# Kernel optimization log

Hardware: AMD Instinct MI355X
Metric: run time of the kernel (lower is better)

Reference implementation:

```python
import jax, jax.numpy as jnp
import numpy as np

IN, H, STEPS = 4, 64, 5

def setup_inputs() -> dict:
    key = jax.random.key(0)
    ks = jax.random.split(key, 12)
    s = 1.0 / np.sqrt(H)
    def u(k, shape):
        return jax.random.uniform(k, shape, jnp.float32, -s, s)
    return {
        "x":    jax.random.normal(ks[0], (4096, 512, IN), jnp.float32),
        "Wih0": u(ks[1], (4 * H, IN)),
        "Whh0": u(ks[2], (4 * H, H)),
        "bih0": u(ks[3], (4 * H,)),
        "bhh0": u(ks[4], (4 * H,)),
        "Wih1": u(ks[5], (4 * H, H)),
        "Whh1": u(ks[6], (4 * H, H)),
        "bih1": u(ks[7], (4 * H,)),
        "bhh1": u(ks[8], (4 * H,)),
        "Wfc":  u(ks[9], (IN * STEPS, H)),
        "bfc":  u(ks[10], (IN * STEPS,)),
    }

def _lstm_layer(x, Wih, Whh, bih, bhh, collect):
    # x: [B, T, in]; PyTorch gate order: i, f, g, o
    B = x.shape[0]
    xg = jnp.einsum('bti,gi->tbg', x, Wih) + bih  # precompute input gates [T,B,4H]
    h0 = jnp.zeros((B, H), x.dtype)
    c0 = jnp.zeros((B, H), x.dtype)

    def step(carry, xg_t):
        h, c = carry
        gates = xg_t + h @ Whh.T + bhh  # [B,4H]
        i, f, g, o = jnp.split(gates, 4, axis=-1)
        i = jax.nn.sigmoid(i); f = jax.nn.sigmoid(f)
        g = jnp.tanh(g);       o = jax.nn.sigmoid(o)
        c = f * c + i * g
        h = o * jnp.tanh(c)
        return (h, c), (h if collect else None)

    (h_last, _), ys = jax.lax.scan(step, (h0, c0), xg)
    return ys, h_last  # ys: [T,B,H] (or None)

def reference(x, Wih0, Whh0, bih0, bhh0, Wih1, Whh1, bih1, bhh1, Wfc, bfc):
    ys1, _ = _lstm_layer(x, Wih0, Whh0, bih0, bhh0, collect=True)   # [T,B,H]
    x2 = jnp.transpose(ys1, (1, 0, 2))                               # [B,T,H]
    _, h_last = _lstm_layer(x2, Wih1, Whh1, bih1, bhh1, collect=False)
    out = h_last @ Wfc.T + bfc                                       # [B, IN*STEPS]
    return out.reshape(-1, STEPS, IN)
```

## Files before the change

### kernel.cpp

```cpp
#include <hip/hip_runtime.h>
#include <cstdint>

#define BLOCK 512
#define BT 16
#define RS_H 136
#define RS_F 68

typedef __attribute__((ext_vector_type(8))) short bf16x8;
typedef __attribute__((ext_vector_type(4))) float f32x4;

#define LOG2E 1.44269504f

static __device__ __forceinline__ float exp2_fast(float x) {
#if __has_builtin(__builtin_amdgcn_exp2f)
    return __builtin_amdgcn_exp2f(x);
#else
    return __expf(x * 0.69314718056f);
#endif
}
static __device__ __forceinline__ float rcp_fast(float x) {
    return __builtin_amdgcn_rcpf(x);
}
static __device__ __forceinline__ unsigned short f2bf(float f) {
    union { float f; unsigned u; } v; v.f = f;
    unsigned r = v.u + 0x7fffu + ((v.u >> 16) & 1u);
    return (unsigned short)(r >> 16);
}
static __device__ __forceinline__ float sigm_y(float y) {
    return rcp_fast(1.0f + exp2_fast(y));
}
static __device__ __forceinline__ float tanh_y(float y) {
    return 1.0f - 2.0f * rcp_fast(exp2_fast(y) + 1.0f);
}
static __device__ __forceinline__ bf16x8 load_wfrag(const float* __restrict__ w, int off, float scale) {
    union { bf16x8 v; unsigned short s[8]; } u;
#pragma unroll
    for (int j = 0; j < 8; ++j) u.s[j] = f2bf(w[off + j] * scale);
    return u.v;
}

extern "C" __global__ void __launch_bounds__(BLOCK, 2)
lstm_fused3(const float* __restrict__ x,
            const float* __restrict__ Wih0, const float* __restrict__ Whh0,
            const float* __restrict__ bih0, const float* __restrict__ bhh0,
            const float* __restrict__ Wih1, const float* __restrict__ Whh1,
            const float* __restrict__ bih1, const float* __restrict__ bhh1,
            const float* __restrict__ Wfc,  const float* __restrict__ bfc,
            float* __restrict__ out)
{
    __shared__ unsigned short hbuf[2][BT * RS_H];
    __shared__ float hfin[BT * RS_F];

    const int tid   = threadIdx.x;
    const int b0    = blockIdx.x * BT;
    const int lane  = tid & 63;
    const int wv    = tid >> 6;
    const int layer = wv >> 2;
    const int cb    = (wv & 3) * 16;
    const int n16   = lane & 15;
    const int quad  = lane >> 4;

    for (int i = tid; i < 2 * BT * RS_H; i += BLOCK)
        ((unsigned short*)hbuf)[i] = 0;

    const float gsc[4] = {-LOG2E, -LOG2E, 2.0f * LOG2E, -LOG2E};

    bf16x8 wf[4][4];
    float bias[4];
    if (layer == 0) {
#pragma unroll
        for (int g = 0; g < 4; ++g) {
            const int gc = g * 64 + cb + n16;
            const float s = gsc[g];
            wf[g][0] = load_wfrag(Whh0 + gc * 64, quad * 8, s);
            wf[g][1] = load_wfrag(Whh0 + gc * 64, 32 + quad * 8, s);
            union { bf16x8 v; unsigned short s_[8]; } u;
#pragma unroll
            for (int c = 0; c < 4; ++c)
                u.s_[c] = (quad == 0) ? f2bf(Wih0[gc * 4 + c] * s) : (unsigned short)0;
            u.s_[4] = 0; u.s_[5] = 0; u.s_[6] = 0; u.s_[7] = 0;
            wf[g][2] = u.v;
            union { bf16x8 v; unsigned short s_[8]; } z;
#pragma unroll
            for (int c = 0; c < 8; ++c) z.s_[c] = 0;
            wf[g][3] = z.v;
            bias[g] = (bih0[gc] + bhh0[gc]) * s;
        }
    } else {
#pragma unroll
        for (int g = 0; g < 4; ++g) {
            const int gc = g * 64 + cb + n16;
            const float s = gsc[g];
            wf[g][0] = load_wfrag(Wih1 + gc * 64, quad * 8, s);
            wf[g][1] = load_wfrag(Wih1 + gc * 64, 32 + quad * 8, s);
            wf[g][2] = load_wfrag(Whh1 + gc * 64, quad * 8, s);
            wf[g][3] = load_wfrag(Whh1 + gc * 64, 32 + quad * 8, s);
            bias[g] = (bih1[gc] + bhh1[gc]) * s;
        }
    }

    float cst[4] = {0.f, 0.f, 0.f, 0.f};

    const f32x4* __restrict__ xrow = (const f32x4*)x + (size_t)(b0 + n16) * 512;
    f32x4 xnext = {0.f, 0.f, 0.f, 0.f};
    if (layer == 0) xnext = xrow[0];

    __syncthreads();

    for (int it = 0; it <= 512; ++it) {
        const unsigned short* rb = &hbuf[(it + 1) & 1][0];
        unsigned short*       wb = &hbuf[it & 1][0];

        const f32x4 xcur = xnext;
        if (layer == 0 && it < 511) xnext = xrow[it + 1];

        bf16x8 a0 = *(const bf16x8*)(rb + n16 * RS_H + quad * 8);
        bf16x8 a1 = *(const bf16x8*)(rb + n16 * RS_H + 32 + quad * 8);
        bf16x8 a2, a3;
        if (layer == 0) {
            union { bf16x8 v; unsigned short s[8]; } u;
            u.s[0] = (quad == 0) ? f2bf(xcur[0]) : (unsigned short)0;
            u.s[1] = (quad == 0) ? f2bf(xcur[1]) : (unsigned short)0;
            u.s[2] = (quad == 0) ? f2bf(xcur[2]) : (unsigned short)0;
            u.s[3] = (quad == 0) ? f2bf(xcur[3]) : (unsigned short)0;
            u.s[4] = 0; u.s[5] = 0; u.s[6] = 0; u.s[7] = 0;
            a2 = u.v;
            a3 = u.v;
        } else {
            a2 = *(const bf16x8*)(rb + n16 * RS_H + 64 + quad * 8);
            a3 = *(const bf16x8*)(rb + n16 * RS_H + 96 + quad * 8);
        }

        f32x4 acc[4];
#pragma unroll
        for (int g = 0; g < 4; ++g) {
            acc[g] = (f32x4){bias[g], bias[g], bias[g], bias[g]};
            acc[g] = __builtin_amdgcn_mfma_f32_16x16x32_bf16(a0, wf[g][0], acc[g], 0, 0, 0);
            acc[g] = __builtin_amdgcn_mfma_f32_16x16x32_bf16(a1, wf[g][1], acc[g], 0, 0, 0);
            acc[g] = __builtin_amdgcn_mfma_f32_16x16x32_bf16(a2, wf[g][2], acc[g], 0, 0, 0);
            acc[g] = __builtin_amdgcn_mfma_f32_16x16x32_bf16(a3, wf[g][3], acc[g], 0, 0, 0);
        }

        const bool active = layer ? (it >= 1) : (it < 512);
        if (active) {
#pragma unroll
            for (int r = 0; r < 4; ++r) {
                const float iv = sigm_y(acc[0][r]);
                const float fv = sigm_y(acc[1][r]);
                const float gv = tanh_y(acc[2][r]);
                const float ov = sigm_y(acc[3][r]);
                const float cc = fv * cst[r] + iv * gv;
                cst[r] = cc;
                const float hh = ov * tanh_y(cc * (2.0f * LOG2E));
                const int row = quad * 4 + r;
                wb[row * RS_H + layer * 64 + cb + n16] = f2bf(hh);
                if (layer == 1 && it == 512) hfin[row * RS_F + cb + n16] = hh;
            }
        }
        __syncthreads();
    }

    if (tid < BT * 20) {
        const int m = tid / 20, k = tid % 20;
        float acc = bfc[k];
#pragma unroll 8
        for (int j = 0; j < 64; ++j)
            acc += hfin[m * RS_F + j] * Wfc[k * 64 + j];
        out[(b0 + m) * 20 + k] = acc;
    }
}

extern "C" void kernel_launch(void* const* d_in, const int* in_sizes, int n_in,
                              void* d_out, int out_size, void* d_ws, size_t ws_size,
                              hipStream_t stream)
{
    (void)in_sizes; (void)n_in; (void)d_ws; (void)ws_size; (void)out_size;
    const float* xp    = (const float*)d_in[0];
    const float* Wih0p = (const float*)d_in[1];
    const float* Whh0p = (const float*)d_in[2];
    const float* bih0p = (const float*)d_in[3];
    const float* bhh0p = (const float*)d_in[4];
    const float* Wih1p = (const float*)d_in[5];
    const float* Whh1p = (const float*)d_in[6];
    const float* bih1p = (const float*)d_in[7];
    const float* bhh1p = (const float*)d_in[8];
    const float* Wfcp  = (const float*)d_in[9];
    const float* bfcp  = (const float*)d_in[10];

    lstm_fused3<<<dim3(256), dim3(BLOCK), 0, stream>>>(
        xp, Wih0p, Whh0p, bih0p, bhh0p, Wih1p, Whh1p, bih1p, bhh1p,
        Wfcp, bfcp, (float*)d_out);
}
```

Baseline: 508.4 us.

## Stage bf16 x tile in LDS, drop zero MFMA, prescale cell state

Preloads the block's whole input sequence into shared memory as bf16 before the recurrence, so each step reads x from LDS instead of issuing a global load and converting per step. Layer 0 skips its fourth MFMA per gate, which only multiplied zeros. Bias is fed directly as the MFMA accumulator, and the cell state is kept prescaled by 2*log2e so the tanh activations fold into FMAs. The x tile adds about 64KB of LDS per block, which may limit the two-blocks-per-CU occupancy the launch bounds target.

```diff
diff --git a/kernel.cpp b/kernel.cpp
--- a/kernel.cpp
+++ b/kernel.cpp
@@ -5,9 +5,11 @@
 #define BT 16
 #define RS_H 136
 #define RS_F 68
+#define XS   2052
 
 typedef __attribute__((ext_vector_type(8))) short bf16x8;
 typedef __attribute__((ext_vector_type(4))) float f32x4;
+typedef __attribute__((ext_vector_type(2))) unsigned int u32x2;
 
 #define LOG2E 1.44269504f
 
@@ -29,9 +31,6 @@
 static __device__ __forceinline__ float sigm_y(float y) {
     return rcp_fast(1.0f + exp2_fast(y));
 }
-static __device__ __forceinline__ float tanh_y(float y) {
-    return 1.0f - 2.0f * rcp_fast(exp2_fast(y) + 1.0f);
-}
 static __device__ __forceinline__ bf16x8 load_wfrag(const float* __restrict__ w, int off, float scale) {
     union { bf16x8 v; unsigned short s[8]; } u;
 #pragma unroll
@@ -40,7 +39,7 @@
 }
 
 extern "C" __global__ void __launch_bounds__(BLOCK, 2)
-lstm_fused3(const float* __restrict__ x,
+lstm_fused4(const float* __restrict__ x,
             const float* __restrict__ Wih0, const float* __restrict__ Whh0,
             const float* __restrict__ bih0, const float* __restrict__ bhh0,
             const float* __restrict__ Wih1, const float* __restrict__ Whh1,
@@ -50,6 +49,7 @@
 {
     __shared__ unsigned short hbuf[2][BT * RS_H];
     __shared__ float hfin[BT * RS_F];
+    __shared__ unsigned short xlds[BT * XS + 8];
 
     const int tid   = threadIdx.x;
     const int b0    = blockIdx.x * BT;
@@ -63,10 +63,22 @@
     for (int i = tid; i < 2 * BT * RS_H; i += BLOCK)
         ((unsigned short*)hbuf)[i] = 0;
 
+    for (int i = tid; i < BT * 512; i += BLOCK) {
+        const int r = i >> 9, t = i & 511;
+        const f32x4 xv = *(const f32x4*)(x + ((size_t)(b0 + r) * 2048 + t * 4));
+        const unsigned lo = (unsigned)f2bf(xv[0]) | ((unsigned)f2bf(xv[1]) << 16);
+        const unsigned hi = (unsigned)f2bf(xv[2]) | ((unsigned)f2bf(xv[3]) << 16);
+        *(u32x2*)&xlds[r * XS + t * 4] = (u32x2){lo, hi};
+    }
+    if (tid <= BT) {
+        const int off = (tid < BT) ? tid * XS + 2048 : BT * XS;
+        *(u32x2*)&xlds[off] = (u32x2){0u, 0u};
+    }
+
     const float gsc[4] = {-LOG2E, -LOG2E, 2.0f * LOG2E, -LOG2E};
 
     bf16x8 wf[4][4];
-    float bias[4];
+    f32x4  biasv[4];
     if (layer == 0) {
 #pragma unroll
         for (int g = 0; g < 4; ++g) {
@@ -80,11 +92,8 @@
                 u.s_[c] = (quad == 0) ? f2bf(Wih0[gc * 4 + c] * s) : (unsigned short)0;
             u.s_[4] = 0; u.s_[5] = 0; u.s_[6] = 0; u.s_[7] = 0;
             wf[g][2] = u.v;
-            union { bf16x8 v; unsigned short s_[8]; } z;
-#pragma unroll
-            for (int c = 0; c < 8; ++c) z.s_[c] = 0;
-            wf[g][3] = z.v;
-            bias[g] = (bih0[gc] + bhh0[gc]) * s;
+            const float b = (bih0[gc] + bhh0[gc]) * s;
+            biasv[g] = (f32x4){b, b, b, b};
         }
     } else {
 #pragma unroll
@@ -95,15 +104,16 @@
             wf[g][1] = load_wfrag(Wih1 + gc * 64, 32 + quad * 8, s);
             wf[g][2] = load_wfrag(Whh1 + gc * 64, quad * 8, s);
             wf[g][3] = load_wfrag(Whh1 + gc * 64, 32 + quad * 8, s);
-            bias[g] = (bih1[gc] + bhh1[gc]) * s;
+            const float b = (bih1[gc] + bhh1[gc]) * s;
+            biasv[g] = (f32x4){b, b, b, b};
         }
     }
 
     float cst[4] = {0.f, 0.f, 0.f, 0.f};
 
-    const f32x4* __restrict__ xrow = (const f32x4*)x + (size_t)(b0 + n16) * 512;
-    f32x4 xnext = {0.f, 0.f, 0.f, 0.f};
-    if (layer == 0) xnext = xrow[0];
+    int xoff = (quad == 0) ? n16 * XS : BT * XS;
+    const int xadv = (quad == 0) ? 4 : 0;
+    const int rbase = n16 * RS_H;
 
     __syncthreads();
 
@@ -111,34 +121,32 @@
         const unsigned short* rb = &hbuf[(it + 1) & 1][0];
         unsigned short*       wb = &hbuf[it & 1][0];
 
-        const f32x4 xcur = xnext;
-        if (layer == 0 && it < 511) xnext = xrow[it + 1];
-
-        bf16x8 a0 = *(const bf16x8*)(rb + n16 * RS_H + quad * 8);
-        bf16x8 a1 = *(const bf16x8*)(rb + n16 * RS_H + 32 + quad * 8);
-        bf16x8 a2, a3;
+        const bf16x8 a0 = *(const bf16x8*)(rb + rbase + quad * 8);
+        const bf16x8 a1 = *(const bf16x8*)(rb + rbase + 32 + quad * 8);
+
+        f32x4 acc[4];
         if (layer == 0) {
-            union { bf16x8 v; unsigned short s[8]; } u;
-            u.s[0] = (quad == 0) ? f2bf(xcur[0]) : (unsigned short)0;
-            u.s[1] = (quad == 0) ? f2bf(xcur[1]) : (unsigned short)0;
-            u.s[2] = (quad == 0) ? f2bf(xcur[2]) : (unsigned short)0;
-            u.s[3] = (quad == 0) ? f2bf(xcur[3]) : (unsigned short)0;
-            u.s[4] = 0; u.s[5] = 0; u.s[6] = 0; u.s[7] = 0;
-            a2 = u.v;
-            a3 = u.v;
+            const u32x2 xr = *(const u32x2*)&xlds[xoff];
+            xoff += xadv;
+            union { bf16x8 v; unsigned u[4]; } ax;
+            ax.u[0] = xr.x; ax.u[1] = xr.y; ax.u[2] = 0u; ax.u[3] = 0u;
+            const bf16x8 a2 = ax.v;
+#pragma unroll
+            for (int g = 0; g < 4; ++g) {
+                acc[g] = __builtin_amdgcn_mfma_f32_16x16x32_bf16(a0, wf[g][0], biasv[g], 0, 0, 0);
+                acc[g] = __builtin_amdgcn_mfma_f32_16x16x32_bf16(a1, wf[g][1], acc[g], 0, 0, 0);
+                acc[g] = __builtin_amdgcn_mfma_f32_16x16x32_bf16(a2, wf[g][2], acc[g], 0, 0, 0);
+            }
         } else {
-            a2 = *(const bf16x8*)(rb + n16 * RS_H + 64 + quad * 8);
-            a3 = *(const bf16x8*)(rb + n16 * RS_H + 96 + quad * 8);
-        }
-
-        f32x4 acc[4];
-#pragma unroll
-        for (int g = 0; g < 4; ++g) {
-            acc[g] = (f32x4){bias[g], bias[g], bias[g], bias[g]};
-            acc[g] = __builtin_amdgcn_mfma_f32_16x16x32_bf16(a0, wf[g][0], acc[g], 0, 0, 0);
-            acc[g] = __builtin_amdgcn_mfma_f32_16x16x32_bf16(a1, wf[g][1], acc[g], 0, 0, 0);
-            acc[g] = __builtin_amdgcn_mfma_f32_16x16x32_bf16(a2, wf[g][2], acc[g], 0, 0, 0);
-            acc[g] = __builtin_amdgcn_mfma_f32_16x16x32_bf16(a3, wf[g][3], acc[g], 0, 0, 0);
+            const bf16x8 a2 = *(const bf16x8*)(rb + rbase + 64 + quad * 8);
+            const bf16x8 a3 = *(const bf16x8*)(rb + rbase + 96 + quad * 8);
+#pragma unroll
+            for (int g = 0; g < 4; ++g) {
+                acc[g] = __builtin_amdgcn_mfma_f32_16x16x32_bf16(a0, wf[g][0], biasv[g], 0, 0, 0);
+                acc[g] = __builtin_amdgcn_mfma_f32_16x16x32_bf16(a1, wf[g][1], acc[g], 0, 0, 0);
+                acc[g] = __builtin_amdgcn_mfma_f32_16x16x32_bf16(a2, wf[g][2], acc[g], 0, 0, 0);
+                acc[g] = __builtin_amdgcn_mfma_f32_16x16x32_bf16(a3, wf[g][3], acc[g], 0, 0, 0);
+            }
         }
 
         const bool active = layer ? (it >= 1) : (it < 512);
@@ -147,11 +155,13 @@
             for (int r = 0; r < 4; ++r) {
                 const float iv = sigm_y(acc[0][r]);
                 const float fv = sigm_y(acc[1][r]);
-                const float gv = tanh_y(acc[2][r]);
+                const float rg = rcp_fast(exp2_fast(acc[2][r]) + 1.0f);
+                const float g2 = fmaf(rg, -4.0f * LOG2E, 2.0f * LOG2E);
                 const float ov = sigm_y(acc[3][r]);
-                const float cc = fv * cst[r] + iv * gv;
-                cst[r] = cc;
-                const float hh = ov * tanh_y(cc * (2.0f * LOG2E));
+                const float c2 = fmaf(fv, cst[r], iv * g2);
+                cst[r] = c2;
+                const float rc = rcp_fast(exp2_fast(c2) + 1.0f);
+                const float hh = ov * fmaf(rc, -2.0f, 1.0f);
                 const int row = quad * 4 + r;
                 wb[row * RS_H + layer * 64 + cb + n16] = f2bf(hh);
                 if (layer == 1 && it == 512) hfin[row * RS_F + cb + n16] = hh;
@@ -187,7 +197,7 @@
     const float* Wfcp  = (const float*)d_in[9];
     const float* bfcp  = (const float*)d_in[10];
 
-    lstm_fused3<<<dim3(256), dim3(BLOCK), 0, stream>>>(
+    lstm_fused4<<<dim3(256), dim3(BLOCK), 0, stream>>>(
         xp, Wih0p, Whh0p, bih0p, bhh0p, Wih1p, Whh1p, bih1p, bhh1p,
         Wfcp, bfcp, (float*)d_out);
 }
```

Result: faster. 465.9 us (-8.4%).
